# Optimization experiments

Measured on AMD Instinct MI355X. Metric: run time of the kernel, lower is better.

## Reference

```python
import jax, jax.numpy as jnp
import numpy as np

B, C, L = 8, 256, 2048        # batch, query_dim, seq len
HEADS, DIM_HEAD = 4, 32
HIDDEN = HEADS * DIM_HEAD      # 128
EPS = 1e-05
SCALE = DIM_HEAD ** -0.5


def setup_inputs() -> dict:
    key = jax.random.key(0)
    ks = jax.random.split(key, 8)
    s_in = 1.0 / np.sqrt(C)
    s_h = 1.0 / np.sqrt(HIDDEN)
    return {
        "x": jax.random.normal(ks[0], (B, C, L), dtype=jnp.float32),
        "g": jnp.ones((1, C, 1), dtype=jnp.float32),
        "b": jnp.zeros((1, C, 1), dtype=jnp.float32),
        "Wq": jax.random.normal(ks[1], (HIDDEN, C), dtype=jnp.float32) * s_in,
        "Wk": jax.random.normal(ks[2], (HIDDEN, C), dtype=jnp.float32) * s_in,
        "Wv": jax.random.normal(ks[3], (HIDDEN, C), dtype=jnp.float32) * s_in,
        "Wo": jax.random.normal(ks[4], (C, HIDDEN), dtype=jnp.float32) * s_h,
        "bo": jnp.zeros((C,), dtype=jnp.float32),
    }


def reference(x, g, b, Wq, Wk, Wv, Wo, bo):
    og_x = x
    # channel-dim LayerNorm (dim=1), biased variance
    mean = jnp.mean(x, axis=1, keepdims=True)
    var = jnp.var(x, axis=1, keepdims=True)
    xn = (x - mean) / jnp.sqrt(var + EPS) * g + b          # [B, C, L]
    xt = jnp.transpose(xn, (0, 2, 1))                      # [B, L, C]
    # QKV projections (self-attention: context = normed x)
    q = xt @ Wq.T                                          # [B, L, HIDDEN]
    k = xt @ Wk.T
    v = xt @ Wv.T
    # b (h c) d layout: [B, HEADS, DIM_HEAD, L]
    split = lambda t: jnp.transpose(t, (0, 2, 1)).reshape(B, HEADS, DIM_HEAD, L)
    q, k, v = split(q), split(k), split(v)
    # scores over head-channel dim c -> [B, H, L, L]
    qk = jnp.einsum('bhcd,bhce->bhde', q, k) * SCALE
    attn = jax.nn.softmax(qk, axis=-1)
    out = jnp.einsum('bhde,bhce->bhcd', attn, v)           # [B, H, DIM_HEAD, L]
    out = out.reshape(B, HIDDEN, L)
    # 1x1 Conv1d: hidden -> query_dim
    y = jnp.einsum('oc,bcl->bol', Wo, out) + bo[None, :, None]
    return y + og_x
```

## Files before the change

### kernel.cpp

```cpp
#include <hip/hip_runtime.h>
#include <math.h>

#define BB_ 8
#define CC_ 256
#define LL_ 2048
#define HEADS_ 4
#define DHEAD_ 32
#define HID_ 128
#define EPS_ 1e-5f
#define SCALE_ 0.17677669529663687f
#define K1_ (SCALE_ * 1.44269504088896f)

typedef short v8s  __attribute__((ext_vector_type(8)));
typedef float v4f  __attribute__((ext_vector_type(4)));
typedef float v16f __attribute__((ext_vector_type(16)));
typedef unsigned v4u __attribute__((ext_vector_type(4)));

__device__ inline short f2bf(float x) {
    union { float f; unsigned u; } a; a.f = x;
    unsigned r = a.u + 0x7fffu + ((a.u >> 16) & 1u);
    return (short)(r >> 16);
}
__device__ inline unsigned fbits(float x) { union { float f; unsigned u; } a; a.f = x; return a.u; }

__global__ __launch_bounds__(256) void k_prep(
    const float* __restrict__ Wq, const float* __restrict__ Wk, const float* __restrict__ Wv,
    const float* __restrict__ Wo, const float* __restrict__ g, const float* __restrict__ bvec,
    short* __restrict__ wqkv, short* __restrict__ wo, float2* __restrict__ gb)
{
    __shared__ float red0[4], red1[4];
    const int blk = blockIdx.x, c = threadIdx.x;
    const int wave = c >> 6, lane = c & 63;
    if (blk < 384) {
        const float* W; int oo; float scale = 1.f;
        if (blk < 128)      { W = Wq; oo = blk;       scale = K1_; }
        else if (blk < 256) { W = Wk; oo = blk - 128; }
        else                { W = Wv; oo = blk - 256; }
        float w  = W[oo * 256 + c] * scale;
        float wg = w * g[c];
        wqkv[blk * 256 + c] = f2bf(wg);
        float r0 = wg, r1 = w * bvec[c];
        #pragma unroll
        for (int off = 1; off < 64; off <<= 1) {
            r0 += __shfl_xor(r0, off, 64);
            r1 += __shfl_xor(r1, off, 64);
        }
        if (lane == 0) { red0[wave] = r0; red1[wave] = r1; }
        __syncthreads();
        if (c == 0)
            gb[blk] = make_float2(red0[0] + red0[1] + red0[2] + red0[3],
                                  red1[0] + red1[1] + red1[2] + red1[3]);
    } else {
        int i2 = (blk - 384) * 256 + c;
        wo[i2] = f2bf(Wo[i2]);
    }
}

__global__ __launch_bounds__(512) void k_ln_qkv(
    const float* __restrict__ x, const short* __restrict__ wqkv, const float2* __restrict__ gb,
    short* __restrict__ q, short* __restrict__ k, short* __restrict__ v)
{
    __shared__ short xnT[32 * 264];
    __shared__ short st2[128 * 48];
    __shared__ float ps_[8 * 32], ps2_[8 * 32];
    const int b   = blockIdx.y;
    const int l0  = blockIdx.x * 32;
    const int tid = threadIdx.x;
    const int wave = tid >> 6, lane = tid & 63;

    {
        const int ls = tid & 31;
        const int cg = tid >> 5;
        float s = 0.f, s2 = 0.f;
        #pragma unroll
        for (int kk = 0; kk < 8; ++kk) {
            int c = 2 * cg + 32 * kk;
            float t0 = x[((size_t)b * CC_ + c) * LL_ + l0 + ls];
            float t1 = x[((size_t)b * CC_ + c + 1) * LL_ + l0 + ls];
            s += t0 + t1; s2 += t0 * t0 + t1 * t1;
            unsigned pk = (unsigned short)f2bf(t0) | ((unsigned)(unsigned short)f2bf(t1) << 16);
            *(unsigned*)(xnT + ls * 264 + c) = pk;
        }
        s  += __shfl_xor(s, 32, 64);
        s2 += __shfl_xor(s2, 32, 64);
        if (lane < 32) { ps_[wave * 32 + lane] = s; ps2_[wave * 32 + lane] = s2; }
    }
    __syncthreads();

    const int n = lane & 15, quad = lane >> 4;
    const int rowbase = (wave >> 2) * 16;
    const int colbase = (wave & 3) * 96;

    v4f acc[6];
    #pragma unroll
    for (int ct = 0; ct < 6; ++ct) acc[ct] = (v4f){0.f, 0.f, 0.f, 0.f};

    #pragma unroll
    for (int ks = 0; ks < 8; ++ks) {
        const v8s af = *(const v8s*)(xnT + (rowbase + n) * 264 + ks * 32 + quad * 8);
        #pragma unroll
        for (int ct = 0; ct < 6; ++ct) {
            const v8s bfrag = *(const v8s*)(wqkv + (size_t)(colbase + ct * 16 + n) * 256 + ks * 32 + quad * 8);
            acc[ct] = __builtin_amdgcn_mfma_f32_16x16x32_bf16(af, bfrag, acc[ct], 0, 0, 0);
        }
    }
    __syncthreads();

    float rsv[4], rmv[4];
    #pragma unroll
    for (int r = 0; r < 4; ++r) {
        int l = rowbase + quad * 4 + r;
        float s = 0.f, s2 = 0.f;
        #pragma unroll
        for (int p = 0; p < 8; ++p) { s += ps_[p * 32 + l]; s2 += ps2_[p * 32 + l]; }
        float mean = s * (1.f / CC_);
        float var  = s2 * (1.f / CC_) - mean * mean;
        float rs   = rsqrtf(var + EPS_);
        rsv[r] = rs; rmv[r] = rs * mean;
    }
    #pragma unroll
    for (int ct = 0; ct < 6; ++ct) {
        int o = colbase + ct * 16 + n;
        float2 gbo = gb[o];
        #pragma unroll
        for (int r = 0; r < 4; ++r) {
            int l = rowbase + quad * 4 + r;
            float val = rsv[r] * acc[ct][r] - rmv[r] * gbo.x + gbo.y;
            if (o < 256)      xnT[l * 264 + o] = f2bf(val);
            else              st2[(o - 256) * 48 + l] = f2bf(val);
        }
    }
    __syncthreads();

    {
        int u = tid;
        int h = u >> 7, rest = u & 127;
        int l = rest >> 2, dg = rest & 3;
        size_t bh = (size_t)b * HEADS_ + h;
        v8s qv = *(const v8s*)(xnT + l * 264 + h * 32 + dg * 8);
        *(v8s*)(q + (bh * LL_ + l0 + l) * DHEAD_ + dg * 8) = qv;
        v8s kv = *(const v8s*)(xnT + l * 264 + 128 + h * 32 + dg * 8);
        *(v8s*)(k + (bh * LL_ + l0 + l) * DHEAD_ + dg * 8) = kv;

        int op = u >> 2, lg = u & 3;
        v8s vv = *(const v8s*)(st2 + op * 48 + lg * 8);
        int h2 = op >> 5, d = op & 31;
        *(v8s*)(v + (((size_t)b * HEADS_ + h2) * DHEAD_ + d) * LL_ + l0 + lg * 8) = vv;
    }
}

__global__ __launch_bounds__(512) void k_attn(
    const short* __restrict__ q, const short* __restrict__ k, const short* __restrict__ v,
    short* __restrict__ ao)
{
    __shared__ char smem[20480 + 17408 + 512];
    short* Kb     = (short*)smem;
    short* Vb     = (short*)(smem + 20480);
    float* Ost    = (float*)smem;
    float* psumst = (float*)(smem + 20480 + 17408);

    const int linear = blockIdx.y * 16 + blockIdx.x;
    const int cxy = linear & 7, j = linear >> 3;
    const int bh = cxy + 8 * (j >> 4);
    const int qx = j & 15;

    const int b    = bh >> 2, h = bh & 3;
    const int tid  = threadIdx.x;
    const int wave = tid >> 6, lane = tid & 63;
    const int wq   = wave & 3;
    const int kh   = wave >> 2;
    const int m    = lane & 31;
    const int half = lane >> 5;
    const size_t kvbase = (size_t)bh * LL_ * DHEAD_;
    const size_t vbase  = (size_t)bh * DHEAD_ * LL_;

    const int q0 = qx * 128 + wq * 32;

    const v8s qf0 = *(const v8s*)(q + kvbase + (size_t)(q0 + m) * DHEAD_ + half * 8);
    const v8s qf1 = *(const v8s*)(q + kvbase + (size_t)(q0 + m) * DHEAD_ + 16 + half * 8);

    v16f O = {};
    float psum = 0.f;

    const int s_hh  = (tid >> 7) & 1;
    const int s_r   = tid & 127;
    const int s_p   = tid >> 8;
    const int v_hh  = tid >> 8;
    const int v_d   = (tid >> 3) & 31;
    const int v_cg  = tid & 7;

    const short* ksrc0 = k + kvbase + (size_t)(s_hh * 1024 + s_r) * DHEAD_ + s_p * 16;
    const short* vsrc0 = v + vbase + (size_t)v_d * LL_ + v_hh * 1024 + v_cg * 16;
    short* kdst = Kb + s_hh * 5120 + s_r * 40 + s_p * 16;
    short* vdst = Vb + v_hh * 4352 + v_d * 136 + v_cg * 16;

    v8s kr0 = *(const v8s*)(ksrc0);
    v8s kr1 = *(const v8s*)(ksrc0 + 8);
    v8s vr0 = *(const v8s*)(vsrc0);
    v8s vr1 = *(const v8s*)(vsrc0 + 8);

    for (int kc = 0; kc < 1024; kc += 128) {
        __syncthreads();
        *(v8s*)kdst       = kr0;
        *(v8s*)(kdst + 8) = kr1;
        *(v8s*)vdst       = vr0;
        *(v8s*)(vdst + 8) = vr1;
        if (kc < 896) {
            const short* kn = ksrc0 + (size_t)(kc + 128) * DHEAD_;
            const short* vn = vsrc0 + (kc + 128);
            kr0 = *(const v8s*)(kn);
            kr1 = *(const v8s*)(kn + 8);
            vr0 = *(const v8s*)(vn);
            vr1 = *(const v8s*)(vn + 8);
        }
        __syncthreads();

        const short* Kw = Kb + kh * 5120;
        const short* Vw = Vb + kh * 4352;
        #pragma unroll
        for (int ktl = 0; ktl < 128; ktl += 32) {
            const v8s kf0 = *(const v8s*)(Kw + (ktl + m) * 40 + half * 8);
            const v8s kf1 = *(const v8s*)(Kw + (ktl + m) * 40 + 16 + half * 8);
            v16f S = __builtin_amdgcn_mfma_f32_32x32x16_bf16(kf0, qf0, (v16f){}, 0, 0, 0);
            S      = __builtin_amdgcn_mfma_f32_32x32x16_bf16(kf1, qf1, S,        0, 0, 0);

            const v8s vf0 = *(const v8s*)(Vw + m * 136 + ktl + half * 8);
            const v8s vf1 = *(const v8s*)(Vw + m * 136 + ktl + 16 + half * 8);

            unsigned e[8];
            #pragma unroll
            for (int i = 0; i < 8; ++i) {
                float pa = __builtin_amdgcn_exp2f(S[2 * i]);
                float pb = __builtin_amdgcn_exp2f(S[2 * i + 1]);
                psum += pa + pb;
                e[i] = __builtin_amdgcn_perm(fbits(pb) + 0x8000u, fbits(pa) + 0x8000u, 0x07060302u);
            }
            v4u f1, f2;
#if __has_builtin(__builtin_amdgcn_permlane32_swap)
            {
                auto r02 = __builtin_amdgcn_permlane32_swap(e[0], e[2], false, false);
                auto r13 = __builtin_amdgcn_permlane32_swap(e[1], e[3], false, false);
                auto r46 = __builtin_amdgcn_permlane32_swap(e[4], e[6], false, false);
                auto r57 = __builtin_amdgcn_permlane32_swap(e[5], e[7], false, false);
                f1 = (v4u){r02[0], r13[0], r02[1], r13[1]};
                f2 = (v4u){r46[0], r57[0], r46[1], r57[1]};
            }
#else
            {
                unsigned o0 = __shfl_xor(e[0], 32, 64), o1 = __shfl_xor(e[1], 32, 64);
                unsigned o2 = __shfl_xor(e[2], 32, 64), o3 = __shfl_xor(e[3], 32, 64);
                unsigned o4 = __shfl_xor(e[4], 32, 64), o5 = __shfl_xor(e[5], 32, 64);
                unsigned o6 = __shfl_xor(e[6], 32, 64), o7 = __shfl_xor(e[7], 32, 64);
                f1 = half ? (v4u){o2, o3, e[2], e[3]} : (v4u){e[0], e[1], o0, o1};
                f2 = half ? (v4u){o6, o7, e[6], e[7]} : (v4u){e[4], e[5], o4, o5};
            }
#endif
            O = __builtin_amdgcn_mfma_f32_32x32x16_bf16(__builtin_bit_cast(v8s, f1), vf0, O, 0, 0, 0);
            O = __builtin_amdgcn_mfma_f32_32x32x16_bf16(__builtin_bit_cast(v8s, f2), vf1, O, 0, 0, 0);
        }
    }

    psum += __shfl_xor(psum, 32, 64);

    __syncthreads();
    if (kh == 1) {
        #pragma unroll
        for (int r = 0; r < 16; ++r) {
            int qr = (r & 3) + 8 * (r >> 2) + 4 * half;
            Ost[(wq * 32 + qr) * 32 + m] = O[r];
        }
        if (half == 0) psumst[wq * 32 + m] = psum;
    }
    __syncthreads();
    if (kh == 0) {
        float den = psum + psumst[wq * 32 + m];
        float invden = 1.f / den;
        #pragma unroll
        for (int r = 0; r < 16; ++r) {
            int qr = (r & 3) + 8 * (r >> 2) + 4 * half;
            float inv = __shfl(invden, qr, 64);
            float val = (O[r] + Ost[(wq * 32 + qr) * 32 + m]) * inv;
            int row = q0 + qr;
            ao[((size_t)b * LL_ + row) * HID_ + h * DHEAD_ + m] = f2bf(val);
        }
    }
}

__global__ __launch_bounds__(256) void k_oproj(
    const short* __restrict__ ao, const short* __restrict__ wo, const float* __restrict__ bo,
    const float* __restrict__ x, float* __restrict__ out)
{
    const int b = blockIdx.z;
    const int l0 = blockIdx.x * 32;
    const int tid = threadIdx.x;
    const int wave = tid >> 6, lane = tid & 63;
    const int m = lane & 31, half = lane >> 5;
    const int o0 = blockIdx.y * 128 + wave * 32;

    float xv[16]; float bv_[16];
    #pragma unroll
    for (int r = 0; r < 16; ++r) {
        int o = o0 + (r & 3) + 8 * (r >> 2) + 4 * half;
        xv[r]  = x[((size_t)b * CC_ + o) * LL_ + l0 + m];
        bv_[r] = bo[o];
    }

    v8s bf[8];
    #pragma unroll
    for (int ks = 0; ks < 8; ++ks)
        bf[ks] = *(const v8s*)(ao + ((size_t)b * LL_ + l0 + m) * HID_ + ks * 16 + half * 8);

    v16f acc = {};
    #pragma unroll
    for (int ks = 0; ks < 8; ++ks) {
        const v8s af = *(const v8s*)(wo + (size_t)(o0 + m) * HID_ + ks * 16 + half * 8);
        acc = __builtin_amdgcn_mfma_f32_32x32x16_bf16(af, bf[ks], acc, 0, 0, 0);
    }

    #pragma unroll
    for (int r = 0; r < 16; ++r) {
        int o = o0 + (r & 3) + 8 * (r >> 2) + 4 * half;
        size_t oi = ((size_t)b * CC_ + o) * LL_ + l0 + m;
        out[oi] = acc[r] + bv_[r] + xv[r];
    }
}

extern "C" void kernel_launch(void* const* d_in, const int* in_sizes, int n_in,
                              void* d_out, int out_size, void* d_ws, size_t ws_size,
                              hipStream_t stream) {
    const float* x  = (const float*)d_in[0];
    const float* g  = (const float*)d_in[1];
    const float* bv = (const float*)d_in[2];
    const float* Wq = (const float*)d_in[3];
    const float* Wk = (const float*)d_in[4];
    const float* Wv = (const float*)d_in[5];
    const float* Wo = (const float*)d_in[6];
    const float* bo = (const float*)d_in[7];
    float* out = (float*)d_out;

    const size_t qkv_elems = (size_t)BB_ * HEADS_ * LL_ * DHEAD_;
    short* q    = (short*)d_ws;
    short* k    = q + qkv_elems;
    short* v    = k + qkv_elems;
    short* ao   = v + qkv_elems;
    short* wqkv = ao + qkv_elems;
    short* wo   = wqkv + 384 * 256;
    float2* gb  = (float2*)(wo + 256 * 128);

    k_prep  <<<dim3(512), dim3(256), 0, stream>>>(Wq, Wk, Wv, Wo, g, bv, wqkv, wo, gb);
    k_ln_qkv<<<dim3(LL_ / 32, BB_), dim3(512), 0, stream>>>(x, wqkv, gb, q, k, v);
    k_attn  <<<dim3(LL_ / 128, BB_ * HEADS_), dim3(512), 0, stream>>>(q, k, v, ao);
    k_oproj <<<dim3(LL_ / 32, 2, BB_), dim3(256), 0, stream>>>(ao, wo, bo, x, out);
}
```

Before: 145.5 us.

## Double-buffer K/V shared-memory tiles in attention kernel to halve barriers

Splits the K/V shared-memory staging into two buffers, so the next tile is written into the alternate buffer while the current one is consumed. This removes one of the two __syncthreads per 128-key chunk and prefetches two chunks ahead from global memory. The cost is doubled LDS use (about 76KB per block), which may limit occupancy to one block per CU.

Result: no change. 146.3 us (+0.5%).

```diff
diff --git a/kernel.cpp b/kernel.cpp
--- a/kernel.cpp
+++ b/kernel.cpp
@@ -149,15 +149,18 @@
     }
 }
 
+#define BUFS_ 18944
 __global__ __launch_bounds__(512) void k_attn(
     const short* __restrict__ q, const short* __restrict__ k, const short* __restrict__ v,
     short* __restrict__ ao)
 {
-    __shared__ char smem[20480 + 17408 + 512];
-    short* Kb     = (short*)smem;
-    short* Vb     = (short*)(smem + 20480);
+    __shared__ char smem[2 * 37888 + 512];
+    short* Kb0    = (short*)smem;
+    short* Vb0    = (short*)(smem + 20480);
+    short* Kb1    = (short*)(smem + 37888);
+    short* Vb1    = (short*)(smem + 37888 + 20480);
     float* Ost    = (float*)smem;
-    float* psumst = (float*)(smem + 20480 + 17408);
+    float* psumst = (float*)(smem + 2 * 37888);
 
     const int linear = blockIdx.y * 16 + blockIdx.x;
     const int cxy = linear & 7, j = linear >> 3;
@@ -191,32 +194,39 @@
 
     const short* ksrc0 = k + kvbase + (size_t)(s_hh * 1024 + s_r) * DHEAD_ + s_p * 16;
     const short* vsrc0 = v + vbase + (size_t)v_d * LL_ + v_hh * 1024 + v_cg * 16;
-    short* kdst = Kb + s_hh * 5120 + s_r * 40 + s_p * 16;
-    short* vdst = Vb + v_hh * 4352 + v_d * 136 + v_cg * 16;
-
-    v8s kr0 = *(const v8s*)(ksrc0);
-    v8s kr1 = *(const v8s*)(ksrc0 + 8);
-    v8s vr0 = *(const v8s*)(vsrc0);
-    v8s vr1 = *(const v8s*)(vsrc0 + 8);
+    short* kdst0 = Kb0 + s_hh * 5120 + s_r * 40 + s_p * 16;
+    short* vdst0 = Vb0 + v_hh * 4352 + v_d * 136 + v_cg * 16;
+    short* kdst1 = kdst0 + BUFS_;
+    short* vdst1 = vdst0 + BUFS_;
+
+    {
+        v8s a0 = *(const v8s*)(ksrc0), a1 = *(const v8s*)(ksrc0 + 8);
+        v8s b0 = *(const v8s*)(vsrc0), b1 = *(const v8s*)(vsrc0 + 8);
+        *(v8s*)kdst0 = a0; *(v8s*)(kdst0 + 8) = a1;
+        *(v8s*)vdst0 = b0; *(v8s*)(vdst0 + 8) = b1;
+    }
+    v8s kr0 = *(const v8s*)(ksrc0 + (size_t)128 * DHEAD_);
+    v8s kr1 = *(const v8s*)(ksrc0 + (size_t)128 * DHEAD_ + 8);
+    v8s vr0 = *(const v8s*)(vsrc0 + 128);
+    v8s vr1 = *(const v8s*)(vsrc0 + 128 + 8);
+    __syncthreads();
 
     for (int kc = 0; kc < 1024; kc += 128) {
-        __syncthreads();
-        *(v8s*)kdst       = kr0;
-        *(v8s*)(kdst + 8) = kr1;
-        *(v8s*)vdst       = vr0;
-        *(v8s*)(vdst + 8) = vr1;
+        const int cur = (kc >> 7) & 1;
         if (kc < 896) {
-            const short* kn = ksrc0 + (size_t)(kc + 128) * DHEAD_;
-            const short* vn = vsrc0 + (kc + 128);
-            kr0 = *(const v8s*)(kn);
-            kr1 = *(const v8s*)(kn + 8);
-            vr0 = *(const v8s*)(vn);
-            vr1 = *(const v8s*)(vn + 8);
-        }
-        __syncthreads();
-
-        const short* Kw = Kb + kh * 5120;
-        const short* Vw = Vb + kh * 4352;
+            short* kd = cur ? kdst0 : kdst1;
+            short* vd = cur ? vdst0 : vdst1;
+            *(v8s*)kd = kr0; *(v8s*)(kd + 8) = kr1;
+            *(v8s*)vd = vr0; *(v8s*)(vd + 8) = vr1;
+            if (kc < 768) {
+                const short* kn = ksrc0 + (size_t)(kc + 256) * DHEAD_;
+                const short* vn = vsrc0 + (kc + 256);
+                kr0 = *(const v8s*)(kn); kr1 = *(const v8s*)(kn + 8);
+                vr0 = *(const v8s*)(vn); vr1 = *(const v8s*)(vn + 8);
+            }
+        }
+        const short* Kw = (cur ? Kb1 : Kb0) + kh * 5120;
+        const short* Vw = (cur ? Vb1 : Vb0) + kh * 4352;
         #pragma unroll
         for (int ktl = 0; ktl < 128; ktl += 32) {
             const v8s kf0 = *(const v8s*)(Kw + (ktl + m) * 40 + half * 8);
@@ -258,11 +268,11 @@
             O = __builtin_amdgcn_mfma_f32_32x32x16_bf16(__builtin_bit_cast(v8s, f1), vf0, O, 0, 0, 0);
             O = __builtin_amdgcn_mfma_f32_32x32x16_bf16(__builtin_bit_cast(v8s, f2), vf1, O, 0, 0, 0);
         }
+        __syncthreads();
     }
 
     psum += __shfl_xor(psum, 32, 64);
 
-    __syncthreads();
     if (kh == 1) {
         #pragma unroll
         for (int r = 0; r < 16; ++r) {
```
